# Kernel tuning notes

Hardware: AMD Instinct MI355X
Metric: run time of the kernel (lower is better)

## Reference

```python
import jax, jax.numpy as jnp
import numpy as np

L_SPAN = 8          # max event span length
MAX_ITER = 3        # args.max_iteration + 1
RATE = 0.3          # confidence threshold for edge creation
BETA_INTRA = 0.7
BETA_INTER = 0.3


def setup_inputs() -> dict:
    key = jax.random.key(0)
    ks = jax.random.split(key, 16)
    n_sents, S, D = 64, 512, 768
    E, P, NL, H, C = 2000, 20000, 128, 512, 3
    sc = lambda fan: 1.0 / np.sqrt(fan)
    return {
        'sent_emb': jax.random.normal(ks[0], (n_sents, S, D), jnp.float32),
        'W_proj': jax.random.normal(ks[1], (D, NL), jnp.float32) * sc(D),
        'W1': jax.random.normal(ks[2], (2 * D + NL, H), jnp.float32) * sc(2 * D + NL),
        'b1': jnp.zeros((H,), jnp.float32),
        'W2': jax.random.normal(ks[3], (H, C), jnp.float32) * sc(H),
        'b2': jnp.zeros((C,), jnp.float32),
        'W_self': jax.random.normal(ks[4], (NL, NL), jnp.float32) * sc(NL),
        'W_intra': jax.random.normal(ks[5], (NL, NL), jnp.float32) * sc(NL),
        'W_inter': jax.random.normal(ks[6], (NL, NL), jnp.float32) * sc(NL),
        'event_sent': jax.random.randint(ks[7], (E,), 0, n_sents, jnp.int32),
        'event_start': jax.random.randint(ks[8], (E,), 0, S - L_SPAN, jnp.int32),
        'event_len': jax.random.randint(ks[9], (E,), 0, L_SPAN, jnp.int32),
        'pair1': jax.random.randint(ks[10], (P,), 0, E, jnp.int32),
        'pair2': jax.random.randint(ks[11], (P,), 0, E, jnp.int32),
        'rel_type': jax.random.randint(ks[12], (P,), 0, 2, jnp.int32),
        'target': jax.random.randint(ks[13], (P,), 0, 3, jnp.int32),
    }


def _extract_events(sent_emb, event_sent, event_start, event_len):
    # ragged span mean: spans have length 1..L_SPAN
    S = sent_emb.shape[1]
    lens = (event_len + 1).astype(sent_emb.dtype)            # [E]
    offs = jnp.arange(L_SPAN)
    idx = jnp.clip(event_start[:, None] + offs[None, :], 0, S - 1)  # [E, L]
    tok = sent_emb[event_sent[:, None], idx]                 # [E, L, D] gather
    mask = (offs[None, :] < (event_len + 1)[:, None]).astype(sent_emb.dtype)
    return (tok * mask[:, :, None]).sum(1) / lens[:, None]   # [E, D]


def reference(sent_emb, W_proj, W1, b1, W2, b2, W_self, W_intra, W_inter,
              event_sent, event_start, event_len, pair1, pair2, rel_type, target):
    E = event_sent.shape[0]
    e_emb = _extract_events(sent_emb, event_sent, event_start, event_len)   # [E, 768]
    event_pair_embed = jnp.concatenate([e_emb[pair1], e_emb[pair2]], axis=-1)  # [P, 1536]
    x = e_emb @ W_proj                                                      # [E, n_last]

    seg = jax.ops.segment_sum
    loss = jnp.float32(0.0)
    logits = None
    for it in range(MAX_ITER):
        diff = x[pair1] - x[pair2]                                          # [P, n_last]
        feats = jnp.concatenate([event_pair_embed, diff], axis=-1)          # [P, 1536+n_last]
        logits = jax.nn.relu(feats @ W1 + b1) @ W2 + b2                     # [P, C]
        logp = jax.nn.log_softmax(logits, axis=-1)
        ce = -jnp.take_along_axis(logp, target[:, None], axis=-1).mean()
        loss = loss + ce / (it + 1)

        # dynamic graph construction from predictions
        p = jax.nn.softmax(logits, axis=-1)
        conf = p.max(-1) > RATE
        argm = p.argmax(-1)
        f = lambda m: jax.lax.stop_gradient(m.astype(x.dtype))[:, None]
        mi1 = f(conf & (argm == 1) & (rel_type == 0))   # intra: pair1 -> pair2
        mi2 = f(conf & (argm == 2) & (rel_type == 0))   # intra reversed
        me1 = f(conf & (argm == 1) & (rel_type == 1))   # inter
        me2 = f(conf & (argm == 2) & (rel_type == 1))

        # intra aggregation (includes self-loop)
        s_intra = seg(x[pair1] * mi1, pair2, num_segments=E) + \
                  seg(x[pair2] * mi2, pair1, num_segments=E) + x
        c_intra = seg(mi1[:, 0], pair2, num_segments=E) + \
                  seg(mi2[:, 0], pair1, num_segments=E) + 1.0
        agg_intra = s_intra / c_intra[:, None]

        s_inter = seg(x[pair1] * me1, pair2, num_segments=E) + \
                  seg(x[pair2] * me2, pair1, num_segments=E)
        c_inter = seg(me1[:, 0], pair2, num_segments=E) + \
                  seg(me2[:, 0], pair1, num_segments=E)
        agg_inter = s_inter / jnp.maximum(c_inter, 1.0)[:, None]

        x = jax.nn.relu(x @ W_self + BETA_INTRA * (agg_intra @ W_intra)
                        + BETA_INTER * (agg_inter @ W_inter))
    return loss, logits
```

## Files before the change

kernel.cpp:

```cpp
#include <hip/hip_runtime.h>
#include <hip/hip_bf16.h>


#define D_DIM 768
#define H_DIM 512
#define NL_DIM 128
#define KB 32
#define TM 64
#define TN 64

struct Smem {
    float As[KB][TM + 4];
    float Bs[KB][TN];
};

__device__ __forceinline__ void tile_gemm(
    const float* __restrict__ A, int lda,
    const float* __restrict__ Bt, int ldb,
    int m0, int M, int K, Smem& sm, float acc[4][4], int t)
{
    int tm = t >> 4, tn = t & 15;
    for (int k0 = 0; k0 < K; k0 += KB) {
#pragma unroll
        for (int r = 0; r < 2; ++r) {
            int row = (t >> 3) + 32 * r;
            int c4 = (t & 7) * 4;
            float4 av = make_float4(0.f, 0.f, 0.f, 0.f);
            if (m0 + row < M)
                av = *(const float4*)(A + (size_t)(m0 + row) * lda + k0 + c4);
            sm.As[c4 + 0][row] = av.x;
            sm.As[c4 + 1][row] = av.y;
            sm.As[c4 + 2][row] = av.z;
            sm.As[c4 + 3][row] = av.w;
        }
#pragma unroll
        for (int r = 0; r < 2; ++r) {
            int row = (t >> 4) + 16 * r;
            int c4 = (t & 15) * 4;
            *(float4*)&sm.Bs[row][c4] =
                *(const float4*)(Bt + (size_t)(k0 + row) * ldb + c4);
        }
        __syncthreads();
#pragma unroll
        for (int k = 0; k < KB; ++k) {
            float4 a = *(const float4*)&sm.As[k][tm * 4];
            float4 b = *(const float4*)&sm.Bs[k][tn * 4];
            acc[0][0] += a.x * b.x; acc[0][1] += a.x * b.y; acc[0][2] += a.x * b.z; acc[0][3] += a.x * b.w;
            acc[1][0] += a.y * b.x; acc[1][1] += a.y * b.y; acc[1][2] += a.y * b.z; acc[1][3] += a.y * b.w;
            acc[2][0] += a.z * b.x; acc[2][1] += a.z * b.y; acc[2][2] += a.z * b.z; acc[2][3] += a.z * b.w;
            acc[3][0] += a.w * b.x; acc[3][1] += a.w * b.y; acc[3][2] += a.w * b.z; acc[3][3] += a.w * b.w;
        }
        __syncthreads();
    }
}

__global__ __launch_bounds__(256) void gemm_a12x0(
    const float* __restrict__ e_emb, const float* __restrict__ W1,
    const float* __restrict__ W_proj,
    float* __restrict__ A1, float* __restrict__ A2, float* __restrict__ X0, int M)
{
    __shared__ Smem sm;
    int t = threadIdx.x;
    int bx = blockIdx.x;
    int m0 = blockIdx.y * TM;
    const float* Bt; float* Ct; int ldb, ldc;
    if (bx < 8)       { Bt = W1 + bx * 64;                          ldb = 512; Ct = A1 + bx * 64;        ldc = 512; }
    else if (bx < 16) { Bt = W1 + (size_t)768 * 512 + (bx - 8) * 64; ldb = 512; Ct = A2 + (bx - 8) * 64;  ldc = 512; }
    else              { Bt = W_proj + (bx - 16) * 64;               ldb = 128; Ct = X0 + (bx - 16) * 64; ldc = 128; }
    float acc[4][4] = {};
    tile_gemm(e_emb, D_DIM, Bt, ldb, m0, M, D_DIM, sm, acc, t);
    int tm = t >> 4, tn = t & 15;
#pragma unroll
    for (int i = 0; i < 4; ++i) {
        int row = m0 + tm * 4 + i;
        if (row < M)
            *(float4*)(Ct + (size_t)row * ldc + tn * 4) =
                make_float4(acc[i][0], acc[i][1], acc[i][2], acc[i][3]);
    }
}

__global__ __launch_bounds__(256) void gemm_y_uv(
    const float* __restrict__ x, const float* __restrict__ W1k,
    const float* __restrict__ A1, const float* __restrict__ A2,
    const float* __restrict__ b1,
    float* __restrict__ U, float* __restrict__ V, int M)
{
    __shared__ Smem sm;
    int t = threadIdx.x;
    int n0 = blockIdx.x * TN;
    int m0 = blockIdx.y * TM;
    float acc[4][4] = {};
    tile_gemm(x, NL_DIM, W1k + n0, H_DIM, m0, M, NL_DIM, sm, acc, t);
    int tm = t >> 4, tn = t & 15;
    float4 b1v = *(const float4*)(b1 + n0 + tn * 4);
#pragma unroll
    for (int i = 0; i < 4; ++i) {
        int row = m0 + tm * 4 + i;
        if (row < M) {
            size_t off = (size_t)row * H_DIM + n0 + tn * 4;
            float4 a1v = *(const float4*)(A1 + off);
            float4 a2v = *(const float4*)(A2 + off);
            float4 u, v;
            u.x = acc[i][0] + a1v.x + b1v.x;  v.x = a2v.x - acc[i][0];
            u.y = acc[i][1] + a1v.y + b1v.y;  v.y = a2v.y - acc[i][1];
            u.z = acc[i][2] + a1v.z + b1v.z;  v.z = a2v.z - acc[i][2];
            u.w = acc[i][3] + a1v.w + b1v.w;  v.w = a2v.w - acc[i][3];
            *(float4*)(U + off) = u;
            *(float4*)(V + off) = v;
        }
    }
}

__global__ __launch_bounds__(256) void gemm_update3(
    const float* __restrict__ x, const float* __restrict__ aggI, const float* __restrict__ aggE,
    const float* __restrict__ Ws, const float* __restrict__ Wi, const float* __restrict__ We,
    float* __restrict__ xn, int M)
{
    __shared__ Smem sm;
    int t = threadIdx.x;
    int n0 = blockIdx.x * TN;
    int m0 = blockIdx.y * TM;
    float acc[4][4] = {};
    tile_gemm(x,    NL_DIM, Ws + n0, NL_DIM, m0, M, NL_DIM, sm, acc, t);
    tile_gemm(aggI, NL_DIM, Wi + n0, NL_DIM, m0, M, NL_DIM, sm, acc, t);
    tile_gemm(aggE, NL_DIM, We + n0, NL_DIM, m0, M, NL_DIM, sm, acc, t);
    int tm = t >> 4, tn = t & 15;
#pragma unroll
    for (int i = 0; i < 4; ++i) {
        int row = m0 + tm * 4 + i;
        if (row < M)
            *(float4*)(xn + (size_t)row * NL_DIM + n0 + tn * 4) =
                make_float4(fmaxf(acc[i][0], 0.f), fmaxf(acc[i][1], 0.f),
                            fmaxf(acc[i][2], 0.f), fmaxf(acc[i][3], 0.f));
    }
}

__global__ __launch_bounds__(192) void extract_kernel(
    const float* __restrict__ sent_emb, const int* __restrict__ es,
    const int* __restrict__ st, const int* __restrict__ el,
    float* __restrict__ e_emb)
{
    int e = blockIdx.x;
    int t = threadIdx.x;
    int s = es[e];
    int start = st[e];
    int len = el[e] + 1;
    const float* base = sent_emb + ((size_t)s * 512 + start) * D_DIM;
    float4 a = make_float4(0.f, 0.f, 0.f, 0.f);
    for (int k = 0; k < len; ++k) {
        float4 v = ((const float4*)(base + (size_t)k * D_DIM))[t];
        a.x += v.x; a.y += v.y; a.z += v.z; a.w += v.w;
    }
    float inv = 1.0f / (float)len;
    ((float4*)(e_emb + (size_t)e * D_DIM))[t] =
        make_float4(a.x * inv, a.y * inv, a.z * inv, a.w * inv);
}

__global__ __launch_bounds__(256) void zero4_kernel(float4* __restrict__ p, int n4)
{
    int i = blockIdx.x * 256 + threadIdx.x;
    if (i < n4) p[i] = make_float4(0.f, 0.f, 0.f, 0.f);
}

__global__ __launch_bounds__(256) void pair_kernel(
    const float* __restrict__ U, const float* __restrict__ V,
    const float* __restrict__ X, const float* __restrict__ W2,
    const float* __restrict__ b2,
    const int* __restrict__ pair1, const int* __restrict__ pair2,
    const int* __restrict__ rel, const int* __restrict__ tgt,
    float* s_intra, float* s_inter, float* c_intra, float* c_inter,
    float* __restrict__ ce_out, float* logits_out, int P, int do_scatter)
{
    __shared__ float ce_sh[4];
    int t = threadIdx.x;
    int wave = t >> 6;
    int lane = t & 63;
    int base = lane * 8;
    float w2f[24];
    {
        const float4* w2p = (const float4*)(W2 + (size_t)base * 3);
#pragma unroll
        for (int q = 0; q < 6; ++q) *(float4*)&w2f[q * 4] = w2p[q];
    }
    float b20 = b2[0], b21 = b2[1], b22 = b2[2];
    float ce = 0.f;
    int p0 = (blockIdx.x * 4 + wave) * 4;
#pragma unroll
    for (int q = 0; q < 4; ++q) {
        int p = p0 + q;
        if (p >= P) break;
        int p1 = pair1[p], p2 = pair2[p];
        float uf[8], vf[8];
        {
            const float4* up = (const float4*)(U + (size_t)p1 * H_DIM + base);
            const float4* vp = (const float4*)(V + (size_t)p2 * H_DIM + base);
            *(float4*)&uf[0] = up[0]; *(float4*)&uf[4] = up[1];
            *(float4*)&vf[0] = vp[0]; *(float4*)&vf[4] = vp[1];
        }
        float l0 = 0.f, l1 = 0.f, l2 = 0.f;
#pragma unroll
        for (int i = 0; i < 8; ++i) {
            float h = fmaxf(uf[i] + vf[i], 0.f);
            l0 += h * w2f[i * 3 + 0];
            l1 += h * w2f[i * 3 + 1];
            l2 += h * w2f[i * 3 + 2];
        }
#pragma unroll
        for (int off = 32; off > 0; off >>= 1) {
            l0 += __shfl_xor(l0, off);
            l1 += __shfl_xor(l1, off);
            l2 += __shfl_xor(l2, off);
        }
        l0 += b20; l1 += b21; l2 += b22;
        float m = fmaxf(l0, fmaxf(l1, l2));
        float lse = m + logf(expf(l0 - m) + expf(l1 - m) + expf(l2 - m));
        int tg = tgt[p];
        float lt = (tg == 0) ? l0 : ((tg == 1) ? l1 : l2);
        ce += lse - lt;
        if (logits_out && lane == 0) {
            logits_out[(size_t)p * 3 + 0] = l0;
            logits_out[(size_t)p * 3 + 1] = l1;
            logits_out[(size_t)p * 3 + 2] = l2;
        }
        if (do_scatter) {
            int argm = 0; float mx = l0;
            if (l1 > mx) { mx = l1; argm = 1; }
            if (l2 > mx) { mx = l2; argm = 2; }
            if (argm != 0) {
                int r = rel[p];
                int src = (argm == 1) ? p1 : p2;
                int dst = (argm == 1) ? p2 : p1;
                float* sacc = (r == 0) ? s_intra : s_inter;
                float* cacc = (r == 0) ? c_intra : c_inter;
                const float* xs = X + (size_t)src * NL_DIM;
                float* sd = sacc + (size_t)dst * NL_DIM;
                atomicAdd(&sd[lane], xs[lane]);
                atomicAdd(&sd[lane + 64], xs[lane + 64]);
                if (lane == 0) atomicAdd(&cacc[dst], 1.0f);
            }
        }
    }
    if (lane == 0) ce_sh[wave] = ce;
    __syncthreads();
    if (t == 0) ce_out[blockIdx.x] = ce_sh[0] + ce_sh[1] + ce_sh[2] + ce_sh[3];
}

__global__ __launch_bounds__(256) void agg_kernel(
    const float* __restrict__ s_intra, const float* __restrict__ s_inter,
    const float* __restrict__ c_intra, const float* __restrict__ c_inter,
    const float* __restrict__ X,
    float* __restrict__ aggI, float* __restrict__ aggE, int n)
{
    int i = blockIdx.x * 256 + threadIdx.x;
    if (i >= n) return;
    int e = i >> 7;
    float ci = c_intra[e] + 1.0f;
    float cf = fmaxf(c_inter[e], 1.0f);
    aggI[i] = 0.7f * (s_intra[i] + X[i]) / ci;
    aggE[i] = 0.3f * s_inter[i] / cf;
}

__global__ __launch_bounds__(256) void loss_kernel(
    const float* __restrict__ ce, int nblk, int P, float* __restrict__ out)
{
    int t = threadIdx.x;
    float acc = 0.f;
    for (int it = 0; it < 3; ++it) {
        float w = 1.0f / ((float)P * (float)(it + 1));
        for (int i = t; i < nblk; i += 256)
            acc += ce[(size_t)it * nblk + i] * w;
    }
    __shared__ float red[256];
    red[t] = acc;
    __syncthreads();
    for (int s = 128; s > 0; s >>= 1) {
        if (t < s) red[t] += red[t + s];
        __syncthreads();
    }
    if (t == 0) out[0] = red[0];
}

extern "C" void kernel_launch(void* const* d_in, const int* in_sizes, int n_in,
                              void* d_out, int out_size, void* d_ws, size_t ws_size,
                              hipStream_t stream)
{
    const float* sent_emb  = (const float*)d_in[0];
    const float* W_proj    = (const float*)d_in[1];
    const float* W1        = (const float*)d_in[2];
    const float* b1        = (const float*)d_in[3];
    const float* W2        = (const float*)d_in[4];
    const float* b2        = (const float*)d_in[5];
    const float* W_self    = (const float*)d_in[6];
    const float* W_intra   = (const float*)d_in[7];
    const float* W_inter   = (const float*)d_in[8];
    const int* event_sent  = (const int*)d_in[9];
    const int* event_start = (const int*)d_in[10];
    const int* event_len   = (const int*)d_in[11];
    const int* pair1       = (const int*)d_in[12];
    const int* pair2       = (const int*)d_in[13];
    const int* rel_type    = (const int*)d_in[14];
    const int* target      = (const int*)d_in[15];

    int E = in_sizes[9];
    int P = in_sizes[12];
    float* out = (float*)d_out;
    float* ws  = (float*)d_ws;

    size_t o = 0;
    float* e_emb   = ws + o; o += (size_t)E * D_DIM;
    float* A1      = ws + o; o += (size_t)E * H_DIM;
    float* A2      = ws + o; o += (size_t)E * H_DIM;
    float* V       = ws + o; o += (size_t)E * H_DIM;
    float* X0      = ws + o; o += (size_t)E * NL_DIM;
    float* X1      = ws + o; o += (size_t)E * NL_DIM;
    float* s_intra = ws + o; o += (size_t)E * NL_DIM;
    float* s_inter = ws + o; o += (size_t)E * NL_DIM;
    float* c_intra = ws + o; o += (size_t)E;
    float* c_inter = ws + o; o += (size_t)E;
    float* aggI    = ws + o; o += (size_t)E * NL_DIM;
    float* aggE    = ws + o; o += (size_t)E * NL_DIM;
    int NBLK = (P + 15) / 16;
    float* ceb     = ws + o; o += (size_t)3 * NBLK;
    float* U       = e_emb;

    extract_kernel<<<E, 192, 0, stream>>>(sent_emb, event_sent, event_start, event_len, e_emb);

    dim3 gF(18, (E + TM - 1) / TM);
    gemm_a12x0<<<gF, 256, 0, stream>>>(e_emb, W1, W_proj, A1, A2, X0, E);

    const float* W1k = W1 + (size_t)2 * D_DIM * H_DIM;
    dim3 gY(H_DIM / TN, (E + TM - 1) / TM);
    dim3 gU(NL_DIM / TN, (E + TM - 1) / TM);
    float* xcur = X0;
    float* xnext = X1;
    int zn4 = (E * NL_DIM * 2 + E * 2) / 4;
    for (int it = 0; it < 3; ++it) {
        int last = (it == 2);
        gemm_y_uv<<<gY, 256, 0, stream>>>(xcur, W1k, A1, A2, b1, U, V, E);
        if (!last)
            zero4_kernel<<<(zn4 + 255) / 256, 256, 0, stream>>>((float4*)s_intra, zn4);
        pair_kernel<<<NBLK, 256, 0, stream>>>(U, V, xcur, W2, b2,
                                              pair1, pair2, rel_type, target,
                                              s_intra, s_inter, c_intra, c_inter,
                                              ceb + (size_t)it * NBLK,
                                              last ? (out + 1) : nullptr, P, !last);
        if (!last) {
            agg_kernel<<<(E * NL_DIM + 255) / 256, 256, 0, stream>>>(
                s_intra, s_inter, c_intra, c_inter, xcur, aggI, aggE, E * NL_DIM);
            gemm_update3<<<gU, 256, 0, stream>>>(xcur, aggI, aggE, W_self, W_intra, W_inter, xnext, E);
            float* tmp = xcur; xcur = xnext; xnext = tmp;
        }
    }
    loss_kernel<<<1, 256, 0, stream>>>(ceb, NBLK, P, out);
}
```

Measured before the change: 470.0 us.

## Split-K double-buffered 128-row GEMM with atomic accumulation; prefetch pair gathers

Replaces the first projection GEMM with a 128x64 tile, register-prefetched double-buffered kernel that splits K four ways across blockIdx.z and accumulates into zeroed outputs with atomics. A1, A2 and X0 are made contiguous so a single zero kernel clears them first. The pair kernel now loads all four pairs' indices and U/V rows up front to overlap gather latency. The atomics add extra memory traffic and make results nondeterministic, and the extra zero launch adds work.

```diff
diff --git a/kernel.cpp b/kernel.cpp
--- a/kernel.cpp
+++ b/kernel.cpp
@@ -5,6 +5,119 @@
 #define D_DIM 768
 #define H_DIM 512
 #define NL_DIM 128
+
+#define FTM 128
+#define FTN 64
+#define FKB 32
+#define FKZ 4
+
+__global__ __launch_bounds__(256) void gemm_fused(
+    const float* __restrict__ Ag, const float* __restrict__ W1,
+    const float* __restrict__ W_proj,
+    float* __restrict__ A1, float* __restrict__ A2, float* __restrict__ X0, int M)
+{
+    __shared__ float As[2][FKB][FTM + 4];
+    __shared__ float Bs[2][FKB][FTN];
+    int t = threadIdx.x;
+    int bx = blockIdx.x;
+    int m0 = blockIdx.y * FTM;
+    int kbase = blockIdx.z * (D_DIM / FKZ);
+    const float* Bt; float* Ct; int ldb, ldc;
+    if (bx < 8)       { Bt = W1 + bx * 64;                           ldb = 512; Ct = A1 + bx * 64;        ldc = 512; }
+    else if (bx < 16) { Bt = W1 + (size_t)768 * 512 + (bx - 8) * 64; ldb = 512; Ct = A2 + (bx - 8) * 64;  ldc = 512; }
+    else              { Bt = W_proj + (bx - 16) * 64;                ldb = 128; Ct = X0 + (bx - 16) * 64; ldc = 128; }
+
+    int ar  = t >> 3;
+    int ac4 = (t & 7) * 4;
+    int br  = t >> 4;
+    int bc4 = (t & 15) * 4;
+    int tm  = t >> 4;
+    int tn  = t & 15;
+
+    float acc[8][4] = {};
+    const int NT = (D_DIM / FKZ) / FKB;
+    float4 pa[4], pb[2];
+
+#pragma unroll
+    for (int p = 0; p < 4; ++p) {
+        int row = m0 + ar + 32 * p;
+        pa[p] = (row < M) ? *(const float4*)(Ag + (size_t)row * D_DIM + kbase + ac4)
+                          : make_float4(0.f, 0.f, 0.f, 0.f);
+    }
+#pragma unroll
+    for (int p = 0; p < 2; ++p)
+        pb[p] = *(const float4*)(Bt + (size_t)(kbase + br + 16 * p) * ldb + bc4);
+#pragma unroll
+    for (int p = 0; p < 4; ++p) {
+        As[0][ac4 + 0][ar + 32 * p] = pa[p].x;
+        As[0][ac4 + 1][ar + 32 * p] = pa[p].y;
+        As[0][ac4 + 2][ar + 32 * p] = pa[p].z;
+        As[0][ac4 + 3][ar + 32 * p] = pa[p].w;
+    }
+#pragma unroll
+    for (int p = 0; p < 2; ++p)
+        *(float4*)&Bs[0][br + 16 * p][bc4] = pb[p];
+    __syncthreads();
+
+    for (int kt = 0; kt < NT; ++kt) {
+        int b = kt & 1;
+        if (kt + 1 < NT) {
+            int k0 = kbase + (kt + 1) * FKB;
+#pragma unroll
+            for (int p = 0; p < 4; ++p) {
+                int row = m0 + ar + 32 * p;
+                pa[p] = (row < M) ? *(const float4*)(Ag + (size_t)row * D_DIM + k0 + ac4)
+                                  : make_float4(0.f, 0.f, 0.f, 0.f);
+            }
+#pragma unroll
+            for (int p = 0; p < 2; ++p)
+                pb[p] = *(const float4*)(Bt + (size_t)(k0 + br + 16 * p) * ldb + bc4);
+        }
+#pragma unroll
+        for (int k = 0; k < FKB; ++k) {
+            float4 a0 = *(const float4*)&As[b][k][tm * 4];
+            float4 a1 = *(const float4*)&As[b][k][64 + tm * 4];
+            float4 bv = *(const float4*)&Bs[b][k][tn * 4];
+            acc[0][0] += a0.x * bv.x; acc[0][1] += a0.x * bv.y; acc[0][2] += a0.x * bv.z; acc[0][3] += a0.x * bv.w;
+            acc[1][0] += a0.y * bv.x; acc[1][1] += a0.y * bv.y; acc[1][2] += a0.y * bv.z; acc[1][3] += a0.y * bv.w;
+            acc[2][0] += a0.z * bv.x; acc[2][1] += a0.z * bv.y; acc[2][2] += a0.z * bv.z; acc[2][3] += a0.z * bv.w;
+            acc[3][0] += a0.w * bv.x; acc[3][1] += a0.w * bv.y; acc[3][2] += a0.w * bv.z; acc[3][3] += a0.w * bv.w;
+            acc[4][0] += a1.x * bv.x; acc[4][1] += a1.x * bv.y; acc[4][2] += a1.x * bv.z; acc[4][3] += a1.x * bv.w;
+            acc[5][0] += a1.y * bv.x; acc[5][1] += a1.y * bv.y; acc[5][2] += a1.y * bv.z; acc[5][3] += a1.y * bv.w;
+            acc[6][0] += a1.z * bv.x; acc[6][1] += a1.z * bv.y; acc[6][2] += a1.z * bv.z; acc[6][3] += a1.z * bv.w;
+            acc[7][0] += a1.w * bv.x; acc[7][1] += a1.w * bv.y; acc[7][2] += a1.w * bv.z; acc[7][3] += a1.w * bv.w;
+        }
+        if (kt + 1 < NT) {
+            int nb = (kt + 1) & 1;
+#pragma unroll
+            for (int p = 0; p < 4; ++p) {
+                As[nb][ac4 + 0][ar + 32 * p] = pa[p].x;
+                As[nb][ac4 + 1][ar + 32 * p] = pa[p].y;
+                As[nb][ac4 + 2][ar + 32 * p] = pa[p].z;
+                As[nb][ac4 + 3][ar + 32 * p] = pa[p].w;
+            }
+#pragma unroll
+            for (int p = 0; p < 2; ++p)
+                *(float4*)&Bs[nb][br + 16 * p][bc4] = pb[p];
+        }
+        __syncthreads();
+    }
+#pragma unroll
+    for (int half = 0; half < 2; ++half) {
+#pragma unroll
+        for (int i = 0; i < 4; ++i) {
+            int row = m0 + half * 64 + tm * 4 + i;
+            if (row < M) {
+                float* cp = Ct + (size_t)row * ldc + tn * 4;
+                atomicAdd(&cp[0], acc[half * 4 + i][0]);
+                atomicAdd(&cp[1], acc[half * 4 + i][1]);
+                atomicAdd(&cp[2], acc[half * 4 + i][2]);
+                atomicAdd(&cp[3], acc[half * 4 + i][3]);
+            }
+        }
+    }
+}
+
 #define KB 32
 #define TM 64
 #define TN 64
@@ -51,31 +164,6 @@
             acc[3][0] += a.w * b.x; acc[3][1] += a.w * b.y; acc[3][2] += a.w * b.z; acc[3][3] += a.w * b.w;
         }
         __syncthreads();
-    }
-}
-
-__global__ __launch_bounds__(256) void gemm_a12x0(
-    const float* __restrict__ e_emb, const float* __restrict__ W1,
-    const float* __restrict__ W_proj,
-    float* __restrict__ A1, float* __restrict__ A2, float* __restrict__ X0, int M)
-{
-    __shared__ Smem sm;
-    int t = threadIdx.x;
-    int bx = blockIdx.x;
-    int m0 = blockIdx.y * TM;
-    const float* Bt; float* Ct; int ldb, ldc;
-    if (bx < 8)       { Bt = W1 + bx * 64;                          ldb = 512; Ct = A1 + bx * 64;        ldc = 512; }
-    else if (bx < 16) { Bt = W1 + (size_t)768 * 512 + (bx - 8) * 64; ldb = 512; Ct = A2 + (bx - 8) * 64;  ldc = 512; }
-    else              { Bt = W_proj + (bx - 16) * 64;               ldb = 128; Ct = X0 + (bx - 16) * 64; ldc = 128; }
-    float acc[4][4] = {};
-    tile_gemm(e_emb, D_DIM, Bt, ldb, m0, M, D_DIM, sm, acc, t);
-    int tm = t >> 4, tn = t & 15;
-#pragma unroll
-    for (int i = 0; i < 4; ++i) {
-        int row = m0 + tm * 4 + i;
-        if (row < M)
-            *(float4*)(Ct + (size_t)row * ldc + tn * 4) =
-                make_float4(acc[i][0], acc[i][1], acc[i][2], acc[i][3]);
     }
 }
 
@@ -183,24 +271,33 @@
         for (int q = 0; q < 6; ++q) *(float4*)&w2f[q * 4] = w2p[q];
     }
     float b20 = b2[0], b21 = b2[1], b22 = b2[2];
+    int p0 = (blockIdx.x * 4 + wave) * 4;
+
+    int pi1[4], pi2[4];
+#pragma unroll
+    for (int q = 0; q < 4; ++q) {
+        int p = min(p0 + q, P - 1);
+        pi1[q] = pair1[p];
+        pi2[q] = pair2[p];
+    }
+    float uf[4][8], vf[4][8];
+#pragma unroll
+    for (int q = 0; q < 4; ++q) {
+        const float4* up = (const float4*)(U + (size_t)pi1[q] * H_DIM + base);
+        const float4* vp = (const float4*)(V + (size_t)pi2[q] * H_DIM + base);
+        *(float4*)&uf[q][0] = up[0]; *(float4*)&uf[q][4] = up[1];
+        *(float4*)&vf[q][0] = vp[0]; *(float4*)&vf[q][4] = vp[1];
+    }
+
     float ce = 0.f;
-    int p0 = (blockIdx.x * 4 + wave) * 4;
 #pragma unroll
     for (int q = 0; q < 4; ++q) {
         int p = p0 + q;
         if (p >= P) break;
-        int p1 = pair1[p], p2 = pair2[p];
-        float uf[8], vf[8];
-        {
-            const float4* up = (const float4*)(U + (size_t)p1 * H_DIM + base);
-            const float4* vp = (const float4*)(V + (size_t)p2 * H_DIM + base);
-            *(float4*)&uf[0] = up[0]; *(float4*)&uf[4] = up[1];
-            *(float4*)&vf[0] = vp[0]; *(float4*)&vf[4] = vp[1];
-        }
         float l0 = 0.f, l1 = 0.f, l2 = 0.f;
 #pragma unroll
         for (int i = 0; i < 8; ++i) {
-            float h = fmaxf(uf[i] + vf[i], 0.f);
+            float h = fmaxf(uf[q][i] + vf[q][i], 0.f);
             l0 += h * w2f[i * 3 + 0];
             l1 += h * w2f[i * 3 + 1];
             l2 += h * w2f[i * 3 + 2];
@@ -228,8 +325,8 @@
             if (l2 > mx) { mx = l2; argm = 2; }
             if (argm != 0) {
                 int r = rel[p];
-                int src = (argm == 1) ? p1 : p2;
-                int dst = (argm == 1) ? p2 : p1;
+                int src = (argm == 1) ? pi1[q] : pi2[q];
+                int dst = (argm == 1) ? pi2[q] : pi1[q];
                 float* sacc = (r == 0) ? s_intra : s_inter;
                 float* cacc = (r == 0) ? c_intra : c_inter;
                 const float* xs = X + (size_t)src * NL_DIM;
@@ -310,8 +407,8 @@
     float* e_emb   = ws + o; o += (size_t)E * D_DIM;
     float* A1      = ws + o; o += (size_t)E * H_DIM;
     float* A2      = ws + o; o += (size_t)E * H_DIM;
+    float* X0      = ws + o; o += (size_t)E * NL_DIM;
     float* V       = ws + o; o += (size_t)E * H_DIM;
-    float* X0      = ws + o; o += (size_t)E * NL_DIM;
     float* X1      = ws + o; o += (size_t)E * NL_DIM;
     float* s_intra = ws + o; o += (size_t)E * NL_DIM;
     float* s_inter = ws + o; o += (size_t)E * NL_DIM;
@@ -323,10 +420,12 @@
     float* ceb     = ws + o; o += (size_t)3 * NBLK;
     float* U       = e_emb;
 
+    int cz4 = E * (H_DIM * 2 + NL_DIM) / 4;
+    zero4_kernel<<<(cz4 + 255) / 256, 256, 0, stream>>>((float4*)A1, cz4);
     extract_kernel<<<E, 192, 0, stream>>>(sent_emb, event_sent, event_start, event_len, e_emb);
 
-    dim3 gF(18, (E + TM - 1) / TM);
-    gemm_a12x0<<<gF, 256, 0, stream>>>(e_emb, W1, W_proj, A1, A2, X0, E);
+    dim3 gF(18, (E + FTM - 1) / FTM, FKZ);
+    gemm_fused<<<gF, 256, 0, stream>>>(e_emb, W1, W_proj, A1, A2, X0, E);
 
     const float* W1k = W1 + (size_t)2 * D_DIM * H_DIM;
     dim3 gY(H_DIM / TN, (E + TM - 1) / TM);
```

New measurement: 537.0 us. 14.3% more time.
